# Kernel tuning notes

Hardware: AMD Instinct MI355X
Metric: run time of the kernel (lower is better)

## Reference

```python
import jax, jax.numpy as jnp
import numpy as np

MARGIN = 0.5
EPS = 1e-6  # torch F.pairwise_distance adds eps to the difference before the norm
B, N, D = 1024, 1024, 64


def setup_inputs() -> dict:
    key = jax.random.key(0)
    ka, kp, kn = jax.random.split(key, 3)
    anchor = jax.random.normal(ka, (B, N, D), dtype=jnp.float32)
    positive = jax.random.normal(kp, (B, N, D), dtype=jnp.float32)
    negative = jax.random.normal(kn, (B, N, D), dtype=jnp.float32)
    return {"anchor": anchor, "positive": positive, "negative": negative}


def reference(anchor, positive, negative):
    # pairwise L2 distances over the feature dim -> [B, N]
    dist_pos = jnp.linalg.norm(anchor - positive + EPS, axis=-1)
    dist_neg = jnp.linalg.norm(anchor - negative + EPS, axis=-1)

    # hard-negative mining, vectorized over the batch:
    # candidates are columns where dist_pos - dist_neg + margin > 0;
    # among candidates pick the column with the LARGEST dist_neg
    diff = dist_pos - dist_neg + MARGIN            # [B, N]
    valid = diff > 0                               # [B, N]
    neg_scores = jnp.where(valid, dist_neg, -jnp.inf)
    sel_col = jnp.argmax(neg_scores, axis=1)       # [B] column index of hard negative

    # faithful to the original: negative is indexed on its FIRST dim with the
    # selected column index (requires B == N), yielding [B, N, D]
    hard_neg = negative[sel_col]
    has_valid = jnp.any(valid, axis=1)             # rows the original would keep

    loss = jnp.mean(jax.nn.relu(MARGIN + dist_pos - dist_neg))
    return loss, hard_neg, has_valid
```

## Files before the change

kernel.cpp:

```cpp
#include <hip/hip_runtime.h>
#include <math.h>

#define BB 1024
#define NN 1024
#define DD 64
#define MARGIN_V 0.5f
#define EPS_V 1e-6f
#define QSPLIT 4
#define QCOLS (NN / QSPLIT)

typedef float f32x4 __attribute__((ext_vector_type(4)));

__global__ __launch_bounds__(256) void k_dist(const float* __restrict__ a,
                                              const float* __restrict__ p,
                                              const float* __restrict__ g,
                                              float* __restrict__ ws_loss,
                                              float* __restrict__ ws_score,
                                              int* __restrict__ ws_idx,
                                              int* __restrict__ ws_valid)
{
    const int blk  = blockIdx.x;
    const int b    = blk >> 2;
    const int q    = blk & 3;
    const int tid  = threadIdx.x;
    const int lane = tid & 63;
    const int wave = tid >> 6;
    const int grp  = lane >> 4;
    const int gl   = lane & 15;
    const int group = wave * 4 + grp;

    const size_t base  = (size_t)b * (NN * DD);
    const int    ncol0 = q * QCOLS + group;

    float loss_acc   = 0.f;
    float best_score = -INFINITY;
    int   best_idx   = 0x7fffffff;

    #pragma unroll 1
    for (int h = 0; h < 2; ++h) {
        f32x4 va[8], vp[8], vg[8];
        #pragma unroll
        for (int i = 0; i < 8; ++i) {
            const int n = ncol0 + (h * 8 + i) * 16;
            const size_t off = base + (size_t)n * DD + (size_t)gl * 4;
            va[i] = __builtin_nontemporal_load((const f32x4*)(a + off));
            vp[i] = __builtin_nontemporal_load((const f32x4*)(p + off));
            vg[i] = *(const f32x4*)(g + off);
        }

        float accp[8], accn[8];
        #pragma unroll
        for (int i = 0; i < 8; ++i) {
            float sp = 0.f, sn = 0.f, t;
            #pragma unroll
            for (int e = 0; e < 4; ++e) {
                t = va[i][e] - vp[i][e] + EPS_V; sp += t * t;
                t = va[i][e] - vg[i][e] + EPS_V; sn += t * t;
            }
            accp[i] = sp; accn[i] = sn;
        }

        #pragma unroll
        for (int i = 0; i < 8; ++i) {
            #pragma unroll
            for (int m = 1; m < 16; m <<= 1) {
                accp[i] += __shfl_xor(accp[i], m, 64);
                accn[i] += __shfl_xor(accn[i], m, 64);
            }
        }

        #pragma unroll
        for (int i = 0; i < 8; ++i) {
            if (gl == i) {
                const int n = ncol0 + (h * 8 + i) * 16;
                const float diff = MARGIN_V + sqrtf(accp[i]) - sqrtf(accn[i]);
                loss_acc += fmaxf(diff, 0.f);
                const float sc = (diff > 0.f) ? sqrtf(accn[i]) : -INFINITY;
                if (sc > best_score || (sc == best_score && n < best_idx)) {
                    best_score = sc; best_idx = n;
                }
            }
        }
    }

    for (int m = 1; m < 64; m <<= 1) {
        loss_acc += __shfl_xor(loss_acc, m, 64);
        const float so = __shfl_xor(best_score, m, 64);
        const int   io = __shfl_xor(best_idx, m, 64);
        if (so > best_score || (so == best_score && io < best_idx)) {
            best_score = so; best_idx = io;
        }
    }

    __shared__ float s_loss[4];
    __shared__ float s_score[4];
    __shared__ int   s_idx[4];
    if ((tid & 63) == 0) {
        s_loss[wave]  = loss_acc;
        s_score[wave] = best_score;
        s_idx[wave]   = best_idx;
    }
    __syncthreads();
    if (tid == 0) {
        float ls = 0.f, bs = -INFINITY;
        int   bi = 0x7fffffff;
        for (int k = 0; k < 4; ++k) {
            ls += s_loss[k];
            const float sc = s_score[k]; const int ix = s_idx[k];
            if (sc > bs || (sc == bs && ix < bi)) { bs = sc; bi = ix; }
        }
        ws_loss[blk]  = ls;
        ws_score[blk] = bs;
        ws_idx[blk]   = bi;
        ws_valid[blk] = (bs > -INFINITY) ? 1 : 0;
    }
}

__global__ __launch_bounds__(1024) void k_merge(const float* __restrict__ ws_loss,
                                                const float* __restrict__ ws_score,
                                                const int* __restrict__ ws_idx,
                                                const int* __restrict__ ws_valid,
                                                float* __restrict__ out_loss,
                                                int* __restrict__ ws_sel,
                                                float* __restrict__ out_hasvalid)
{
    const int b = threadIdx.x;
    float ls = 0.f;
    float bs = -INFINITY;
    int   bi = 0x7fffffff;
    int   av = 0;
    for (int qq = 0; qq < QSPLIT; ++qq) {
        const int idx = b * QSPLIT + qq;
        const float sc = ws_score[idx];
        const int   ix = ws_idx[idx];
        if (sc > bs || (sc == bs && ix < bi)) { bs = sc; bi = ix; }
        ls += ws_loss[idx];
        av |= ws_valid[idx];
    }
    ws_sel[b] = bi;
    out_hasvalid[b] = av ? 1.0f : 0.0f;

    __shared__ float s[16];
    float v = ls;
    for (int m = 1; m < 64; m <<= 1) v += __shfl_xor(v, m, 64);
    if ((b & 63) == 0) s[b >> 6] = v;
    __syncthreads();
    if (b == 0) {
        float tot = 0.f;
        for (int k = 0; k < 16; ++k) tot += s[k];
        out_loss[0] = tot / (float)((size_t)BB * NN);
    }
}

__global__ __launch_bounds__(256) void k_gather(const float* __restrict__ g,
                                                const int* __restrict__ ws_sel,
                                                float* __restrict__ out_hn)
{
    const int b   = blockIdx.y;
    const int sel = ws_sel[b];
    const float* __restrict__ src = g      + (size_t)sel * (NN * DD);
    float* __restrict__       dst = out_hn + (size_t)b   * (NN * DD);
    const int t = blockIdx.x * blockDim.x + threadIdx.x;
    #pragma unroll
    for (int k = 0; k < (NN * DD) / 8192; ++k) {
        const int idx = t + k * 8192;
        __builtin_nontemporal_store(src[idx], dst + idx);
    }
}

extern "C" void kernel_launch(void* const* d_in, const int* in_sizes, int n_in,
                              void* d_out, int out_size, void* d_ws, size_t ws_size,
                              hipStream_t stream) {
    const float* anchor   = (const float*)d_in[0];
    const float* positive = (const float*)d_in[1];
    const float* negative = (const float*)d_in[2];
    float* out = (float*)d_out;

    float* out_loss     = out;
    float* out_hard_neg = out + 1;
    float* out_hasvalid = out + 1 + (size_t)BB * NN * DD;

    float* ws_loss  = (float*)d_ws;
    float* ws_score = ws_loss + BB * QSPLIT;
    int*   ws_idx   = (int*)(ws_score + BB * QSPLIT);
    int*   ws_valid = ws_idx + BB * QSPLIT;
    int*   ws_sel   = ws_valid + BB * QSPLIT;

    k_dist<<<dim3(BB * QSPLIT), dim3(256), 0, stream>>>(anchor, positive, negative,
                                                        ws_loss, ws_score, ws_idx, ws_valid);
    k_merge<<<dim3(1), dim3(1024), 0, stream>>>(ws_loss, ws_score, ws_idx, ws_valid,
                                                out_loss, ws_sel, out_hasvalid);
    k_gather<<<dim3(32, BB), dim3(256), 0, stream>>>(negative, ws_sel, out_hard_neg);
}
```

Measured before the change: 213.3 us.

## Stream k_dist inputs through LDS with async global_load_lds multi-buffering

Replaces the register-staged batch loads in the distance kernel with per-wave asynchronous global-to-LDS copies using a 4-slot ring buffer and two chunks in flight, synchronised with explicit vmcnt waits. Each wave now owns a contiguous 64-column slice, consumed 4 columns per chunk. The aim is to keep memory requests continuously outstanding with low register pressure, so this bandwidth-bound kernel can use more of HBM bandwidth. It gives up the nontemporal hints on anchor/positive and adds an LDS round trip plus reliance on hand-counted vmcnt values.

```diff
diff --git a/kernel.cpp b/kernel.cpp
--- a/kernel.cpp
+++ b/kernel.cpp
@@ -8,8 +8,11 @@
 #define EPS_V 1e-6f
 #define QSPLIT 4
 #define QCOLS (NN / QSPLIT)
+#define NCHUNK 16
 
 typedef float f32x4 __attribute__((ext_vector_type(4)));
+typedef __attribute__((address_space(1))) const unsigned char glb_u8;
+typedef __attribute__((address_space(3))) unsigned char lds_u8;
 
 __global__ __launch_bounds__(256) void k_dist(const float* __restrict__ a,
                                               const float* __restrict__ p,
@@ -19,6 +22,8 @@
                                               int* __restrict__ ws_idx,
                                               int* __restrict__ ws_valid)
 {
+    __shared__ __align__(16) unsigned char smem[4][4][3][1024];
+
     const int blk  = blockIdx.x;
     const int b    = blk >> 2;
     const int q    = blk & 3;
@@ -27,61 +32,67 @@
     const int wave = tid >> 6;
     const int grp  = lane >> 4;
     const int gl   = lane & 15;
-    const int group = wave * 4 + grp;
-
-    const size_t base  = (size_t)b * (NN * DD);
-    const int    ncol0 = q * QCOLS + group;
+
+    const int wcol0 = q * QCOLS + wave * 64;
+    const size_t baseByte = ((size_t)b * NN * DD + (size_t)wcol0 * DD) * 4u + (size_t)lane * 16u;
+    const unsigned char* aB = (const unsigned char*)a + baseByte;
+    const unsigned char* pB = (const unsigned char*)p + baseByte;
+    const unsigned char* gB = (const unsigned char*)g + baseByte;
 
     float loss_acc   = 0.f;
     float best_score = -INFINITY;
     int   best_idx   = 0x7fffffff;
 
+    auto STAGE = [&](int ch, int buf) {
+        const size_t o = (size_t)ch * 1024u;
+        __builtin_amdgcn_global_load_lds((glb_u8*)(aB + o), (lds_u8*)&smem[wave][buf][0][0], 16, 0, 0);
+        __builtin_amdgcn_global_load_lds((glb_u8*)(pB + o), (lds_u8*)&smem[wave][buf][1][0], 16, 0, 0);
+        __builtin_amdgcn_global_load_lds((glb_u8*)(gB + o), (lds_u8*)&smem[wave][buf][2][0], 16, 0, 0);
+    };
+
+    auto CONSUME = [&](int ch, int buf) {
+        const int off = grp * 256 + gl * 16;
+        const f32x4 va = *(const f32x4*)&smem[wave][buf][0][off];
+        const f32x4 vp = *(const f32x4*)&smem[wave][buf][1][off];
+        const f32x4 vg = *(const f32x4*)&smem[wave][buf][2][off];
+        float sp = 0.f, sn = 0.f, t;
+        #pragma unroll
+        for (int e = 0; e < 4; ++e) {
+            t = va[e] - vp[e] + EPS_V; sp += t * t;
+            t = va[e] - vg[e] + EPS_V; sn += t * t;
+        }
+        #pragma unroll
+        for (int m = 1; m < 16; m <<= 1) {
+            sp += __shfl_xor(sp, m, 64);
+            sn += __shfl_xor(sn, m, 64);
+        }
+        if (gl == ch) {
+            const int n = wcol0 + ch * 4 + grp;
+            const float diff = MARGIN_V + sqrtf(sp) - sqrtf(sn);
+            loss_acc += fmaxf(diff, 0.f);
+            const float sc = (diff > 0.f) ? sqrtf(sn) : -INFINITY;
+            if (sc > best_score || (sc == best_score && n < best_idx)) {
+                best_score = sc; best_idx = n;
+            }
+        }
+    };
+
+    STAGE(0, 0);
+    STAGE(1, 1);
+
     #pragma unroll 1
-    for (int h = 0; h < 2; ++h) {
-        f32x4 va[8], vp[8], vg[8];
-        #pragma unroll
-        for (int i = 0; i < 8; ++i) {
-            const int n = ncol0 + (h * 8 + i) * 16;
-            const size_t off = base + (size_t)n * DD + (size_t)gl * 4;
-            va[i] = __builtin_nontemporal_load((const f32x4*)(a + off));
-            vp[i] = __builtin_nontemporal_load((const f32x4*)(p + off));
-            vg[i] = *(const f32x4*)(g + off);
-        }
-
-        float accp[8], accn[8];
-        #pragma unroll
-        for (int i = 0; i < 8; ++i) {
-            float sp = 0.f, sn = 0.f, t;
-            #pragma unroll
-            for (int e = 0; e < 4; ++e) {
-                t = va[i][e] - vp[i][e] + EPS_V; sp += t * t;
-                t = va[i][e] - vg[i][e] + EPS_V; sn += t * t;
-            }
-            accp[i] = sp; accn[i] = sn;
-        }
-
-        #pragma unroll
-        for (int i = 0; i < 8; ++i) {
-            #pragma unroll
-            for (int m = 1; m < 16; m <<= 1) {
-                accp[i] += __shfl_xor(accp[i], m, 64);
-                accn[i] += __shfl_xor(accn[i], m, 64);
-            }
-        }
-
-        #pragma unroll
-        for (int i = 0; i < 8; ++i) {
-            if (gl == i) {
-                const int n = ncol0 + (h * 8 + i) * 16;
-                const float diff = MARGIN_V + sqrtf(accp[i]) - sqrtf(accn[i]);
-                loss_acc += fmaxf(diff, 0.f);
-                const float sc = (diff > 0.f) ? sqrtf(accn[i]) : -INFINITY;
-                if (sc > best_score || (sc == best_score && n < best_idx)) {
-                    best_score = sc; best_idx = n;
-                }
-            }
-        }
-    }
+    for (int k = 0; k < NCHUNK - 2; ++k) {
+        STAGE(k + 2, (k + 2) & 3);
+        asm volatile("s_waitcnt vmcnt(6)" ::: "memory");
+        __builtin_amdgcn_sched_barrier(0);
+        CONSUME(k, k & 3);
+    }
+    asm volatile("s_waitcnt vmcnt(3)" ::: "memory");
+    __builtin_amdgcn_sched_barrier(0);
+    CONSUME(NCHUNK - 2, (NCHUNK - 2) & 3);
+    asm volatile("s_waitcnt vmcnt(0)" ::: "memory");
+    __builtin_amdgcn_sched_barrier(0);
+    CONSUME(NCHUNK - 1, (NCHUNK - 1) & 3);
 
     for (int m = 1; m < 64; m <<= 1) {
         loss_acc += __shfl_xor(loss_acc, m, 64);
```

Result: slower. 243.5 us (+14.2%).

## Fuse distance, merge and gather into one kernel via atomic last-block election

Applied to the files above, without the earlier changes.

Replaces the three-kernel pipeline (distance, single-block merge, gather) with one fused kernel plus a tiny init kernel. Per-row atomic counters elect the last of the four quarter-blocks for each row, which merges the partial results and copies the selected 256 KB negative row with that block. A global counter elects the final block to reduce the loss. This removes launch gaps and the serial single-block merge, and overlaps the gather with distance work, but a single 256-thread block now does each row's copy, and the tail block's copy can become a latency bottleneck.

```diff
diff --git a/kernel.cpp b/kernel.cpp
--- a/kernel.cpp
+++ b/kernel.cpp
@@ -8,16 +8,29 @@
 #define EPS_V 1e-6f
 #define QSPLIT 4
 #define QCOLS (NN / QSPLIT)
+#define ROWFLOATS (NN * DD)
 
 typedef float f32x4 __attribute__((ext_vector_type(4)));
 
-__global__ __launch_bounds__(256) void k_dist(const float* __restrict__ a,
-                                              const float* __restrict__ p,
-                                              const float* __restrict__ g,
-                                              float* __restrict__ ws_loss,
-                                              float* __restrict__ ws_score,
-                                              int* __restrict__ ws_idx,
-                                              int* __restrict__ ws_valid)
+__global__ __launch_bounds__(1024) void k_init(int* __restrict__ row_cnt,
+                                               int* __restrict__ done_cnt)
+{
+    row_cnt[threadIdx.x] = 0;
+    if (threadIdx.x == 0) done_cnt[0] = 0;
+}
+
+__global__ __launch_bounds__(256) void k_fused(const float* __restrict__ a,
+                                               const float* __restrict__ p,
+                                               const float* __restrict__ g,
+                                               float* __restrict__ ws_loss,
+                                               float* __restrict__ ws_score,
+                                               int* __restrict__ ws_idx,
+                                               int* __restrict__ ws_valid,
+                                               int* __restrict__ row_cnt,
+                                               int* __restrict__ done_cnt,
+                                               float* __restrict__ out_loss,
+                                               float* __restrict__ out_hn,
+                                               float* __restrict__ out_hasvalid)
 {
     const int blk  = blockIdx.x;
     const int b    = blk >> 2;
@@ -95,6 +108,8 @@
     __shared__ float s_loss[4];
     __shared__ float s_score[4];
     __shared__ int   s_idx[4];
+    __shared__ int   s_flags[2];
+    __shared__ int   s_sel;
     if ((tid & 63) == 0) {
         s_loss[wave]  = loss_acc;
         s_score[wave] = best_score;
@@ -113,58 +128,55 @@
         ws_score[blk] = bs;
         ws_idx[blk]   = bi;
         ws_valid[blk] = (bs > -INFINITY) ? 1 : 0;
-    }
-}
-
-__global__ __launch_bounds__(1024) void k_merge(const float* __restrict__ ws_loss,
-                                                const float* __restrict__ ws_score,
-                                                const int* __restrict__ ws_idx,
-                                                const int* __restrict__ ws_valid,
-                                                float* __restrict__ out_loss,
-                                                int* __restrict__ ws_sel,
-                                                float* __restrict__ out_hasvalid)
-{
-    const int b = threadIdx.x;
-    float ls = 0.f;
-    float bs = -INFINITY;
-    int   bi = 0x7fffffff;
-    int   av = 0;
-    for (int qq = 0; qq < QSPLIT; ++qq) {
-        const int idx = b * QSPLIT + qq;
-        const float sc = ws_score[idx];
-        const int   ix = ws_idx[idx];
-        if (sc > bs || (sc == bs && ix < bi)) { bs = sc; bi = ix; }
-        ls += ws_loss[idx];
-        av |= ws_valid[idx];
-    }
-    ws_sel[b] = bi;
-    out_hasvalid[b] = av ? 1.0f : 0.0f;
-
-    __shared__ float s[16];
-    float v = ls;
-    for (int m = 1; m < 64; m <<= 1) v += __shfl_xor(v, m, 64);
-    if ((b & 63) == 0) s[b >> 6] = v;
+
+        __threadfence();
+        const int o = atomicAdd(&row_cnt[b], 1);
+        int lastrow = (o == 3);
+        int sel = 0;
+        if (lastrow) {
+            __threadfence();
+            float mbs = -INFINITY; int mbi = 0x7fffffff; int av = 0;
+            for (int qq = 0; qq < QSPLIT; ++qq) {
+                const int idx = b * QSPLIT + qq;
+                const float sc = ws_score[idx];
+                const int   ix = ws_idx[idx];
+                if (sc > mbs || (sc == mbs && ix < mbi)) { mbs = sc; mbi = ix; }
+                av |= ws_valid[idx];
+            }
+            sel = mbi;
+            out_hasvalid[b] = av ? 1.0f : 0.0f;
+        }
+        const int d = atomicAdd(done_cnt, 1);
+        s_flags[0] = lastrow;
+        s_flags[1] = (d == QSPLIT * BB - 1);
+        s_sel = sel;
+    }
     __syncthreads();
-    if (b == 0) {
-        float tot = 0.f;
-        for (int k = 0; k < 16; ++k) tot += s[k];
-        out_loss[0] = tot / (float)((size_t)BB * NN);
-    }
-}
-
-__global__ __launch_bounds__(256) void k_gather(const float* __restrict__ g,
-                                                const int* __restrict__ ws_sel,
-                                                float* __restrict__ out_hn)
-{
-    const int b   = blockIdx.y;
-    const int sel = ws_sel[b];
-    const float* __restrict__ src = g      + (size_t)sel * (NN * DD);
-    float* __restrict__       dst = out_hn + (size_t)b   * (NN * DD);
-    const int t = blockIdx.x * blockDim.x + threadIdx.x;
-    #pragma unroll
-    for (int k = 0; k < (NN * DD) / 8192; ++k) {
-        const int idx = t + k * 8192;
-        __builtin_nontemporal_store(src[idx], dst + idx);
+
+    if (s_flags[0]) {
+        const float* __restrict__ src = g      + (size_t)s_sel * ROWFLOATS;
+        float* __restrict__       dst = out_hn + (size_t)b    * ROWFLOATS;
+        #pragma unroll 8
+        for (int k2 = 0; k2 < ROWFLOATS / 256; ++k2) {
+            const int i2 = k2 * 256 + tid;
+            __builtin_nontemporal_store(src[i2], dst + i2);
+        }
+    }
+
+    if (s_flags[1]) {
+        __threadfence();
+        __shared__ float s_red[256];
+        float v = 0.f;
+        #pragma unroll
+        for (int j = 0; j < (QSPLIT * BB) / 256; ++j)
+            v += ws_loss[tid * ((QSPLIT * BB) / 256) + j];
+        s_red[tid] = v;
+        __syncthreads();
+        for (int st = 128; st > 0; st >>= 1) {
+            if (tid < st) s_red[tid] += s_red[tid + st];
+            __syncthreads();
+        }
+        if (tid == 0) out_loss[0] = s_red[0] / (float)((size_t)BB * NN);
     }
 }
 
@@ -184,11 +196,12 @@
     float* ws_score = ws_loss + BB * QSPLIT;
     int*   ws_idx   = (int*)(ws_score + BB * QSPLIT);
     int*   ws_valid = ws_idx + BB * QSPLIT;
-    int*   ws_sel   = ws_valid + BB * QSPLIT;
-
-    k_dist<<<dim3(BB * QSPLIT), dim3(256), 0, stream>>>(anchor, positive, negative,
-                                                        ws_loss, ws_score, ws_idx, ws_valid);
-    k_merge<<<dim3(1), dim3(1024), 0, stream>>>(ws_loss, ws_score, ws_idx, ws_valid,
-                                                out_loss, ws_sel, out_hasvalid);
-    k_gather<<<dim3(32, BB), dim3(256), 0, stream>>>(negative, ws_sel, out_hard_neg);
+    int*   row_cnt  = ws_valid + BB * QSPLIT;
+    int*   done_cnt = row_cnt + BB;
+
+    k_init<<<dim3(1), dim3(1024), 0, stream>>>(row_cnt, done_cnt);
+    k_fused<<<dim3(BB * QSPLIT), dim3(256), 0, stream>>>(anchor, positive, negative,
+                                                         ws_loss, ws_score, ws_idx, ws_valid,
+                                                         row_cnt, done_cnt,
+                                                         out_loss, out_hard_neg, out_hasvalid);
 }
```

After: 847.4 us. 3.97x slower.
